# Kernel tuning notes

Measured on AMD Instinct MI355X. Metric: run time of the kernel, lower is better.

## Reference

```python
import jax, jax.numpy as jnp
import numpy as np


def setup_inputs() -> dict:
    key = jax.random.key(0)
    k1, k2 = jax.random.split(key)
    N, C = 2097152, 40
    input = jax.random.normal(k1, (N, C), dtype=jnp.float32)
    raw = jax.random.uniform(k2, (N, C), dtype=jnp.float32)
    # target rows are probability distributions (as in soft-label CE usage)
    target = raw / jnp.sum(raw, axis=-1, keepdims=True)
    return {"input": input, "target": target}


def reference(input, target):
    # Soft-label cross entropy: loss_i = -sum_c target[i,c] * log_softmax(input)[i,c]
    # (equivalent to the per-class looped F.cross_entropy in the original,
    #  but computes log_softmax once). reduction='mean', weight=None.
    logp = jax.nn.log_softmax(input, axis=-1)  # [N, C]
    per_point = -jnp.sum(target * logp, axis=-1)  # [N]
    return jnp.mean(per_point)
```

## Files before the change

kernel.cpp:

```cpp
#include <hip/hip_runtime.h>
#include <math.h>


#define THREADS 256
#define BLOCKS  2048

__global__ __launch_bounds__(THREADS) void ce_partial(
    const float* __restrict__ input,
    const float* __restrict__ target,
    float* __restrict__ partials, int N)
{
    const int tid    = blockIdx.x * blockDim.x + threadIdx.x;
    const int stride = gridDim.x * blockDim.x;

    float acc = 0.f;
    for (int row = tid; row < N; row += stride) {
        const float4* xin = reinterpret_cast<const float4*>(input  + (size_t)row * 40);
        const float4* tin = reinterpret_cast<const float4*>(target + (size_t)row * 40);

        float4 x[10];
        #pragma unroll
        for (int j = 0; j < 10; ++j) x[j] = xin[j];

        float m = x[0].x;
        #pragma unroll
        for (int j = 0; j < 10; ++j)
            m = fmaxf(m, fmaxf(fmaxf(x[j].x, x[j].y), fmaxf(x[j].z, x[j].w)));

        float se = 0.f, dot = 0.f, ts = 0.f;
        #pragma unroll
        for (int j = 0; j < 10; ++j) {
            float4 t = tin[j];
            se  += __expf(x[j].x - m) + __expf(x[j].y - m)
                 + __expf(x[j].z - m) + __expf(x[j].w - m);
            dot += t.x * x[j].x + t.y * x[j].y + t.z * x[j].z + t.w * x[j].w;
            ts  += t.x + t.y + t.z + t.w;
        }
        const float lse = m + __logf(se);
        acc += ts * lse - dot;
    }

    #pragma unroll
    for (int off = 32; off > 0; off >>= 1) acc += __shfl_down(acc, off, 64);

    __shared__ float sdata[THREADS / 64];
    const int lane = threadIdx.x & 63, wid = threadIdx.x >> 6;
    if (lane == 0) sdata[wid] = acc;
    __syncthreads();
    if (threadIdx.x == 0) {
        float s = 0.f;
        #pragma unroll
        for (int w = 0; w < THREADS / 64; ++w) s += sdata[w];
        partials[blockIdx.x] = s;
    }
}

__global__ __launch_bounds__(256) void ce_final(
    const float* __restrict__ partials, float* __restrict__ out,
    int nPartials, float invN)
{
    float acc = 0.f;
    for (int i = threadIdx.x; i < nPartials; i += blockDim.x) acc += partials[i];

    #pragma unroll
    for (int off = 32; off > 0; off >>= 1) acc += __shfl_down(acc, off, 64);

    __shared__ float sdata[4];
    const int lane = threadIdx.x & 63, wid = threadIdx.x >> 6;
    if (lane == 0) sdata[wid] = acc;
    __syncthreads();
    if (threadIdx.x == 0) {
        out[0] = (sdata[0] + sdata[1] + sdata[2] + sdata[3]) * invN;
    }
}

extern "C" void kernel_launch(void* const* d_in, const int* in_sizes, int n_in,
                              void* d_out, int out_size, void* d_ws, size_t ws_size,
                              hipStream_t stream)
{
    const float* input  = (const float*)d_in[0];
    const float* target = (const float*)d_in[1];
    float* out = (float*)d_out;
    float* partials = (float*)d_ws;

    const int C = 40;
    const int N = in_sizes[0] / C;

    ce_partial<<<BLOCKS, THREADS, 0, stream>>>(input, target, partials, N);
    ce_final<<<1, 256, 0, stream>>>(partials, out, BLOCKS, 1.0f / (float)N);
}
```

Baseline: 117.8 us.

## Stage row tiles into LDS with async global_load_lds double buffering

Adds a tiled kernel in which each 128-thread block streams 128-row tiles of input and target into LDS with async direct-to-LDS loads, double buffered so the next tile's fetch overlaps compute on the current one. Global reads become fully coalesced across the block instead of each thread striding through its own 160-byte row. The grid drops to 512 blocks. The old kernel stays as a fallback for shapes that do not divide evenly. This adds barriers, relies on hand-written vmcnt waits, and uses a large LDS footprint that may limit occupancy.

```diff
diff --git a/kernel.cpp b/kernel.cpp
--- a/kernel.cpp
+++ b/kernel.cpp
@@ -2,10 +2,100 @@
 #include <math.h>
 
 
-#define THREADS 256
-#define BLOCKS  2048
+#define ROWS   128
+#define TB     128
+#define NBLK   512
+#define F4ROW  10
+#define TILEF4 (ROWS * F4ROW)
 
-__global__ __launch_bounds__(THREADS) void ce_partial(
+__device__ __forceinline__ void async_ld16(void* lds, const void* g) {
+    __builtin_amdgcn_global_load_lds(
+        (const __attribute__((address_space(1))) unsigned int*)g,
+        (__attribute__((address_space(3))) unsigned int*)lds,
+        16, 0, 0);
+}
+
+__global__ __launch_bounds__(TB) void ce_tiled(
+    const float* __restrict__ input,
+    const float* __restrict__ target,
+    float* __restrict__ partials, int tilesPerBlock)
+{
+    __shared__ float4 bx[2][TILEF4];
+    __shared__ float4 bt[2][TILEF4];
+
+    const int tid  = threadIdx.x;
+    const int lane = tid & 63;
+    const int w    = tid >> 6;
+    const int tile0 = blockIdx.x * tilesPerBlock;
+
+    const float4* xg = reinterpret_cast<const float4*>(input);
+    const float4* tg = reinterpret_cast<const float4*>(target);
+
+    {
+        const size_t g0 = (size_t)tile0 * TILEF4;
+        #pragma unroll
+        for (int k = 0; k < 10; ++k) {
+            const int idx = (2 * k + w) * 64 + lane;
+            async_ld16(&bx[0][idx], xg + g0 + idx);
+            async_ld16(&bt[0][idx], tg + g0 + idx);
+        }
+    }
+
+    float acc = 0.f;
+    int cur = 0;
+    for (int tt = 0; tt < tilesPerBlock; ++tt) {
+        if (tt + 1 < tilesPerBlock) {
+            const size_t g1 = (size_t)(tile0 + tt + 1) * TILEF4;
+            const int nb = cur ^ 1;
+            #pragma unroll
+            for (int k = 0; k < 10; ++k) {
+                const int idx = (2 * k + w) * 64 + lane;
+                async_ld16(&bx[nb][idx], xg + g1 + idx);
+                async_ld16(&bt[nb][idx], tg + g1 + idx);
+            }
+            asm volatile("s_waitcnt vmcnt(20)" ::: "memory");
+        } else {
+            asm volatile("s_waitcnt vmcnt(0)" ::: "memory");
+        }
+        __builtin_amdgcn_s_barrier();
+
+        const float4* xr = &bx[cur][tid * F4ROW];
+        const float4* tr = &bt[cur][tid * F4ROW];
+
+        float4 x[10];
+        #pragma unroll
+        for (int j = 0; j < 10; ++j) x[j] = xr[j];
+
+        float m = -3.402823466e38f;
+        #pragma unroll
+        for (int j = 0; j < 10; ++j)
+            m = fmaxf(m, fmaxf(fmaxf(x[j].x, x[j].y), fmaxf(x[j].z, x[j].w)));
+
+        float se = 0.f, dot = 0.f, ts = 0.f;
+        #pragma unroll
+        for (int j = 0; j < 10; ++j) {
+            const float4 t = tr[j];
+            se  += __expf(x[j].x - m) + __expf(x[j].y - m)
+                 + __expf(x[j].z - m) + __expf(x[j].w - m);
+            dot += t.x * x[j].x + t.y * x[j].y + t.z * x[j].z + t.w * x[j].w;
+            ts  += t.x + t.y + t.z + t.w;
+        }
+        acc += ts * (m + __logf(se)) - dot;
+
+        asm volatile("s_waitcnt lgkmcnt(0)" ::: "memory");
+        __builtin_amdgcn_s_barrier();
+        cur ^= 1;
+    }
+
+    #pragma unroll
+    for (int off = 32; off > 0; off >>= 1) acc += __shfl_down(acc, off, 64);
+    float* red = reinterpret_cast<float*>(&bx[0][0]);
+    if (lane == 0) red[w] = acc;
+    __syncthreads();
+    if (tid == 0) partials[blockIdx.x] = red[0] + red[1];
+}
+
+__global__ __launch_bounds__(256) void ce_partial(
     const float* __restrict__ input,
     const float* __restrict__ target,
     float* __restrict__ partials, int N)
@@ -17,42 +107,33 @@
     for (int row = tid; row < N; row += stride) {
         const float4* xin = reinterpret_cast<const float4*>(input  + (size_t)row * 40);
         const float4* tin = reinterpret_cast<const float4*>(target + (size_t)row * 40);
-
         float4 x[10];
         #pragma unroll
         for (int j = 0; j < 10; ++j) x[j] = xin[j];
-
-        float m = x[0].x;
+        float m = -3.402823466e38f;
         #pragma unroll
         for (int j = 0; j < 10; ++j)
             m = fmaxf(m, fmaxf(fmaxf(x[j].x, x[j].y), fmaxf(x[j].z, x[j].w)));
-
         float se = 0.f, dot = 0.f, ts = 0.f;
         #pragma unroll
         for (int j = 0; j < 10; ++j) {
-            float4 t = tin[j];
+            const float4 t = tin[j];
             se  += __expf(x[j].x - m) + __expf(x[j].y - m)
                  + __expf(x[j].z - m) + __expf(x[j].w - m);
             dot += t.x * x[j].x + t.y * x[j].y + t.z * x[j].z + t.w * x[j].w;
             ts  += t.x + t.y + t.z + t.w;
         }
-        const float lse = m + __logf(se);
-        acc += ts * lse - dot;
+        acc += ts * (m + __logf(se)) - dot;
     }
 
     #pragma unroll
     for (int off = 32; off > 0; off >>= 1) acc += __shfl_down(acc, off, 64);
-
-    __shared__ float sdata[THREADS / 64];
+    __shared__ float sdata[4];
     const int lane = threadIdx.x & 63, wid = threadIdx.x >> 6;
     if (lane == 0) sdata[wid] = acc;
     __syncthreads();
-    if (threadIdx.x == 0) {
-        float s = 0.f;
-        #pragma unroll
-        for (int w = 0; w < THREADS / 64; ++w) s += sdata[w];
-        partials[blockIdx.x] = s;
-    }
+    if (threadIdx.x == 0)
+        partials[blockIdx.x] = sdata[0] + sdata[1] + sdata[2] + sdata[3];
 }
 
 __global__ __launch_bounds__(256) void ce_final(
@@ -61,17 +142,14 @@
 {
     float acc = 0.f;
     for (int i = threadIdx.x; i < nPartials; i += blockDim.x) acc += partials[i];
-
     #pragma unroll
     for (int off = 32; off > 0; off >>= 1) acc += __shfl_down(acc, off, 64);
-
     __shared__ float sdata[4];
     const int lane = threadIdx.x & 63, wid = threadIdx.x >> 6;
     if (lane == 0) sdata[wid] = acc;
     __syncthreads();
-    if (threadIdx.x == 0) {
+    if (threadIdx.x == 0)
         out[0] = (sdata[0] + sdata[1] + sdata[2] + sdata[3]) * invN;
-    }
 }
 
 extern "C" void kernel_launch(void* const* d_in, const int* in_sizes, int n_in,
@@ -85,7 +163,14 @@
 
     const int C = 40;
     const int N = in_sizes[0] / C;
+    const int totalTiles = N / ROWS;
 
-    ce_partial<<<BLOCKS, THREADS, 0, stream>>>(input, target, partials, N);
-    ce_final<<<1, 256, 0, stream>>>(partials, out, BLOCKS, 1.0f / (float)N);
+    if (N % ROWS == 0 && totalTiles % NBLK == 0) {
+        ce_tiled<<<NBLK, TB, 0, stream>>>(input, target, partials,
+                                          totalTiles / NBLK);
+        ce_final<<<1, 256, 0, stream>>>(partials, out, NBLK, 1.0f / (float)N);
+    } else {
+        ce_partial<<<2048, 256, 0, stream>>>(input, target, partials, N);
+        ce_final<<<1, 256, 0, stream>>>(partials, out, 2048, 1.0f / (float)N);
+    }
 }
```

After: 124.4 us. +5.6%, slower.
